# Performance work log

Measured on AMD Instinct MI355X. Metric: run time of the kernel, lower is better.

Reference implementation:

```python
import jax, jax.numpy as jnp
import numpy as np
from jax import lax

B, N, K, NCP = 4, 2048, 20, 400
EPS = 1e-5


def _bn(x, gamma, beta, axes):
    # training-mode batch norm (biased variance), channel axis = 1
    m = jnp.mean(x, axis=axes, keepdims=True)
    v = jnp.var(x, axis=axes, keepdims=True)
    shape = [1] * x.ndim
    shape[1] = -1
    return (x - m) * lax.rsqrt(v + EPS) * gamma.reshape(shape) + beta.reshape(shape)


def _knn_idx(x, k):
    # x: [B, C, N] -> idx [B, N, k] (nearest, includes self like torch.cdist+topk(largest=False))
    x2 = jnp.sum(x * x, axis=1)  # [B, N]
    d = x2[:, :, None] + x2[:, None, :] - 2.0 * jnp.einsum('bcn,bcm->bnm', x, x)
    return lax.top_k(-d, k)[1]


def _edge_conv(x, w, gamma, beta, k):
    # x: [B, C, N], w: [O, 2C] -> [B, O, N] (1x1 conv + BN + LeakyReLU + max over k)
    idx = _knn_idx(x, k)                      # [B, N, k]
    xt = jnp.transpose(x, (0, 2, 1))          # [B, N, C]
    b = jnp.arange(xt.shape[0])[:, None, None]
    nbr = xt[b, idx]                          # [B, N, k, C]
    ctr = xt[:, :, None, :]
    feat = jnp.concatenate([nbr - ctr, jnp.broadcast_to(ctr, nbr.shape)], axis=-1)  # [B, N, k, 2C]
    y = jnp.einsum('bnkc,oc->bonk', feat, w)  # [B, O, N, k]
    y = jax.nn.leaky_relu(_bn(y, gamma, beta, axes=(0, 2, 3)), 0.2)
    return jnp.max(y, axis=-1)                # [B, O, N]


def setup_inputs() -> dict:
    key = jax.random.key(0)
    ks = jax.random.split(key, 16)
    rnd = lambda k_, s: jax.random.normal(k_, s, dtype=jnp.float32) * 0.02
    inp = {
        'x': jax.random.normal(ks[0], (B, 3, N), dtype=jnp.float32),
        'w1': rnd(ks[1], (64, 6)),    'g1': jnp.ones(64),   'b1': jnp.zeros(64),
        'w2': rnd(ks[2], (128, 128)), 'g2': jnp.ones(128),  'b2': jnp.zeros(128),
        'w3': rnd(ks[3], (256, 256)), 'g3': jnp.ones(256),  'b3': jnp.zeros(256),
        'w4': rnd(ks[4], (512, 512)), 'g4': jnp.ones(512),  'b4': jnp.zeros(512),
        'w5': rnd(ks[5], (2048, 963)), 'g5': jnp.ones(2048), 'b5': jnp.zeros(2048),
        'w6': rnd(ks[6], (2048, 2048)), 'wb6': jnp.zeros(2048), 'g6': jnp.ones(2048), 'b6': jnp.zeros(2048),
        'w7': rnd(ks[7], (4096, 4096)), 'wb7': jnp.zeros(4096), 'g7': jnp.ones(4096), 'b7': jnp.zeros(4096),
        'w8': rnd(ks[8], (NCP, 4096)), 'wb8': jnp.zeros(NCP),
    }
    return inp


def reference(x, w1, g1, b1, w2, g2, b2, w3, g3, b3, w4, g4, b4,
              w5, g5, b5, w6, wb6, g6, b6, w7, wb7, g7, b7, w8, wb8):
    x0 = x                                            # [B, 3, N]
    x1 = _edge_conv(x0, w1, g1, b1, K)                # [B, 64, N]
    x2 = _edge_conv(x1, w2, g2, b2, K)                # [B, 128, N]
    x3 = _edge_conv(x2, w3, g3, b3, K)                # [B, 256, N]
    x4 = _edge_conv(x3, w4, g4, b4, K)                # [B, 512, N]
    h = jnp.concatenate([x0, x1, x2, x3, x4], axis=1) # [B, 963, N]
    h = jnp.einsum('bcn,oc->bon', h, w5)              # [B, 2048, N]
    h = jax.nn.leaky_relu(_bn(h, g5, b5, axes=(0, 2)), 0.2)
    p = jnp.max(h, axis=-1, keepdims=True)            # [B, 2048, 1] global max pool
    y = jnp.einsum('bcl,oc->bol', p, w6) + wb6[None, :, None]
    y = jax.nn.relu(_bn(y, g6, b6, axes=(0, 2)))
    y = jnp.concatenate([y, p], axis=1)               # [B, 4096, 1]
    y = jnp.einsum('bcl,oc->bol', y, w7) + wb7[None, :, None]
    y = jax.nn.relu(_bn(y, g7, b7, axes=(0, 2)))
    y = jnp.einsum('bcl,oc->bol', y, w8) + wb8[None, :, None]
    return jnp.tanh(y[:, :, 0])                       # [B, NCP]
```

## Files before the change

### kernel.cpp

```cpp
#include <hip/hip_runtime.h>
#include <float.h>
#include <math.h>


#define NPTS 2048
#define BATCH 4
#define KNN 20
#define CH_H 963
#define KPAD 992
#define HSTRIDE (CH_H*NPTS)

typedef _Float16 half8 __attribute__((ext_vector_type(8)));
typedef float f32x4 __attribute__((ext_vector_type(4)));

typedef const __attribute__((address_space(1))) unsigned int* gas_p;
typedef __attribute__((address_space(3))) unsigned int* las_p;
__device__ __forceinline__ void gl_lds16(const void* g, void* l){
  __builtin_amdgcn_global_load_lds((gas_p)g, (las_p)l, 16, 0, 0);
}

__device__ __forceinline__ unsigned fenc(float x){
  unsigned u = __float_as_uint(x);
  return (u & 0x80000000u) ? ~u : (u | 0x80000000u);
}
__device__ __forceinline__ float fdec(unsigned u){
  u = (u & 0x80000000u) ? (u ^ 0x80000000u) : ~u;
  return __uint_as_float(u);
}

__global__ void k_convert(const float* __restrict__ x, float* __restrict__ H){
  int i = blockIdx.x*256 + threadIdx.x;
  if (i >= BATCH*3*NPTS) return;
  int b = i / (3*NPTS); int r = i % (3*NPTS);
  H[(size_t)b*HSTRIDE + r] = x[i];
}

__global__ void k_norms(const float* __restrict__ X, int C, float* __restrict__ X2,
                        float* __restrict__ SUMZ){
  int i = blockIdx.x*256 + threadIdx.x;
  if (i < 1024) SUMZ[i] = 0.f;
  int b = i >> 11, n = i & 2047;
  const float* Xb = X + (size_t)b*HSTRIDE + n;
  float s = 0.f;
  for (int c=0;c<C;++c){ float v = Xb[(size_t)c*NPTS]; s = fmaf(v,v,s); }
  X2[i] = s;
}

__global__ __launch_bounds__(256) void k_xsplit(const float* __restrict__ X, int C, int Cpad,
        _Float16* __restrict__ Xhi, _Float16* __restrict__ Xlo)
{
  __shared__ float t[64][65];
  int b = blockIdx.z;
  int n0 = blockIdx.x*64, c0 = blockIdx.y*64;
  int tid = threadIdx.x; int l = tid & 63, m = tid >> 6;
  for (int cc = m; cc < 64; cc += 4){
    int c = c0 + cc;
    t[cc][l] = (c < C) ? X[(size_t)b*HSTRIDE + (size_t)c*NPTS + n0 + l] : 0.f;
  }
  __syncthreads();
  for (int nn = m; nn < 64; nn += 4){
    int c = c0 + l;
    if (c < Cpad){
      float v = t[l][nn];
      _Float16 h = (_Float16)v;
      size_t o = ((size_t)(b<<11)+n0+nn)*Cpad + c;
      Xhi[o] = h;
      Xlo[o] = (_Float16)(v - (float)h);
    }
  }
}

__global__ __launch_bounds__(256) void k_gram(const _Float16* __restrict__ Xhi,
        const _Float16* __restrict__ Xlo, int Cpad, int bbase,
        float* __restrict__ G0, float* __restrict__ G1)
{
  __shared__ half8 AsH[128][4]; __shared__ half8 AsL[128][4];
  __shared__ half8 BsH[128][4]; __shared__ half8 BsL[128][4];
  int bl = blockIdx.z;
  int b  = bbase + bl;
  float* G = bl ? G1 : G0;
  const _Float16* Hb = Xhi + (size_t)(b<<11)*Cpad;
  const _Float16* Lb = Xlo + (size_t)(b<<11)*Cpad;
  int m0 = blockIdx.x*128, n0 = blockIdx.y*128;
  int tid = threadIdx.x;
  int w = tid>>6, lane = tid&63;
  int wm = w>>1, wn = w&1;
  int quad = lane>>4, col = lane&15;
  int wbase = w*128;
  f32x4 acc[4][4];
  #pragma unroll
  for (int i=0;i<4;++i)
    #pragma unroll
    for (int j=0;j<4;++j) acc[i][j] = (f32x4){0.f,0.f,0.f,0.f};

  for (int k0=0; k0<Cpad; k0+=32){
    #pragma unroll
    for (int i=0;i<2;++i){
      int cid = wbase + i*64 + lane;
      int row = cid>>2, kc = cid&3;
      size_t ao = (size_t)(n0+row)*Cpad + k0 + kc*8;
      size_t bo = (size_t)(m0+row)*Cpad + k0 + kc*8;
      int lo = (wbase + i*64)*16;
      gl_lds16(Hb + ao, (char*)AsH + lo);
      gl_lds16(Lb + ao, (char*)AsL + lo);
      gl_lds16(Hb + bo, (char*)BsH + lo);
      gl_lds16(Lb + bo, (char*)BsL + lo);
    }
    __syncthreads();
    half8 ah[4], al[4], bh[4], blo[4];
    #pragma unroll
    for (int mt=0;mt<4;++mt){ ah[mt] = AsH[wm*64 + mt*16 + col][quad];
                              al[mt] = AsL[wm*64 + mt*16 + col][quad]; }
    #pragma unroll
    for (int nt=0;nt<4;++nt){ bh[nt] = BsH[wn*64 + nt*16 + col][quad];
                              blo[nt] = BsL[wn*64 + nt*16 + col][quad]; }
    #pragma unroll
    for (int mt=0;mt<4;++mt)
      #pragma unroll
      for (int nt=0;nt<4;++nt){
        acc[mt][nt] = __builtin_amdgcn_mfma_f32_16x16x32_f16(ah[mt], bh[nt], acc[mt][nt], 0, 0, 0);
        acc[mt][nt] = __builtin_amdgcn_mfma_f32_16x16x32_f16(ah[mt], blo[nt], acc[mt][nt], 0, 0, 0);
        acc[mt][nt] = __builtin_amdgcn_mfma_f32_16x16x32_f16(al[mt], bh[nt], acc[mt][nt], 0, 0, 0);
      }
    __syncthreads();
  }
  #pragma unroll
  for (int mt=0;mt<4;++mt){
    #pragma unroll
    for (int r=0;r<4;++r){
      int n = n0 + wm*64 + mt*16 + quad*4 + r;
      #pragma unroll
      for (int nt=0;nt<4;++nt){
        int m = m0 + wn*64 + nt*16 + col;
        G[(size_t)n*2048 + m] = acc[mt][nt][r];
      }
    }
  }
}

#define KNN_CH(OPC) OPC(0) OPC(1) OPC(2) OPC(3) OPC(4) OPC(5) OPC(6) OPC(7)
#define DECL_CH(ch) float d##ch##_0,d##ch##_1,d##ch##_2,d##ch##_3;
#define LOADG_CH(ch) { float4 g = *(const float4*)(grow + (ch)*256 + base); \
  float4 xm = *(const float4*)(x2b + (ch)*256 + base); \
  d##ch##_0 = x2n + xm.x - 2.f*g.x; d##ch##_1 = x2n + xm.y - 2.f*g.y; \
  d##ch##_2 = x2n + xm.z - 2.f*g.z; d##ch##_3 = x2n + xm.w - 2.f*g.w; }
#define DECL_G(ch) float gv##ch; int gm##ch;
#define MKCH(ch) { gv##ch = d##ch##_0; gm##ch = (ch)*256 + base; \
  if (d##ch##_1 < gv##ch){ gv##ch = d##ch##_1; gm##ch = (ch)*256 + base + 1; } \
  if (d##ch##_2 < gv##ch){ gv##ch = d##ch##_2; gm##ch = (ch)*256 + base + 2; } \
  if (d##ch##_3 < gv##ch){ gv##ch = d##ch##_3; gm##ch = (ch)*256 + base + 3; } }
#define REMCASE(ch) case ch: { \
  if (own){ if (cp==0) d##ch##_0 = FLT_MAX; else if (cp==1) d##ch##_1 = FLT_MAX; \
            else if (cp==2) d##ch##_2 = FLT_MAX; else d##ch##_3 = FLT_MAX; } \
  MKCH(ch) } break;

__global__ __launch_bounds__(256,4) void k_sel(const float* __restrict__ G0,
        const float* __restrict__ G1, const float* __restrict__ X2,
        int bbase, int* __restrict__ IDX)
{
  int tid = threadIdx.x;
  int w = tid >> 6, lane = tid & 63;
  int n = blockIdx.x*4 + w;
  int b = bbase + blockIdx.y;
  const float* grow = (blockIdx.y ? G1 : G0) + (size_t)n*2048;
  const float* x2b  = X2 + (b<<11);
  float x2n = x2b[n];
  int base = lane << 2;
  KNN_CH(DECL_CH)
  KNN_CH(LOADG_CH)
  KNN_CH(DECL_G)
  KNN_CH(MKCH)
  int* op = IDX + ((size_t)(b<<11)+n)*KNN;
  for (int it=0; it<KNN; ++it){
    float v = fminf(fminf(fminf(gv0,gv1),fminf(gv2,gv3)),
                    fminf(fminf(gv4,gv5),fminf(gv6,gv7)));
    #pragma unroll
    for (int s=1; s<64; s<<=1) v = fminf(v, __shfl_xor(v, s));
    int mc = 0x7fffffff;
    mc = (gv7==v) ? gm7 : mc;
    mc = (gv6==v) ? gm6 : mc;
    mc = (gv5==v) ? gm5 : mc;
    mc = (gv4==v) ? gm4 : mc;
    mc = (gv3==v) ? gm3 : mc;
    mc = (gv2==v) ? gm2 : mc;
    mc = (gv1==v) ? gm1 : mc;
    mc = (gv0==v) ? gm0 : mc;
    int m = mc;
    #pragma unroll
    for (int s=1; s<64; s<<=1) m = min(m, __shfl_xor(m, s));
    if (lane==0) op[it] = m;
    int sm = __builtin_amdgcn_readfirstlane(m);
    bool own = (lane == ((sm>>2)&63));
    int cp = sm & 3;
    switch (sm >> 8){ KNN_CH(REMCASE) }
  }
}

__global__ __launch_bounds__(256) void k_vu(const float* __restrict__ X,
        const float* __restrict__ W, int C, int O,
        float* __restrict__ V, float* __restrict__ U)
{
  __shared__ float Xs[8][128];
  __shared__ float Wdv[8][64];
  __shared__ float Wuv[8][64];
  int b = blockIdx.z, n0 = blockIdx.x*128, o0 = blockIdx.y*64;
  int tid = threadIdx.x;
  int tj = tid & 15, ti = tid >> 4;
  float4 aV[8], aU[8];
  #pragma unroll
  for (int i=0;i<8;++i){ aV[i]=make_float4(0,0,0,0); aU[i]=make_float4(0,0,0,0); }
  const float* Xb = X + (size_t)b*HSTRIDE;
  for (int c0=0;c0<C;c0+=8){
    {
      int cc = tid >> 5, nn = (tid & 31) * 4; int c = c0 + cc;
      float4 v = (c<C) ? *(const float4*)(Xb + (size_t)c*NPTS + n0 + nn)
                       : make_float4(0,0,0,0);
      *(float4*)&Xs[cc][nn] = v;
    }
    for (int l=tid;l<512;l+=256){
      int oo=l>>3, cc=l&7, c=c0+cc;
      float wd=0.f, wu=0.f;
      if (c<C){
        const float* wr = W + (size_t)(o0+oo)*(2*C);
        wd = wr[c]; wu = wr[C+c] - wd;
      }
      Wdv[cc][oo]=wd; Wuv[cc][oo]=wu;
    }
    __syncthreads();
    #pragma unroll
    for (int cc=0;cc<8;++cc){
      float4 x0 = *(float4*)&Xs[cc][ti*8];
      float4 x1 = *(float4*)&Xs[cc][ti*8+4];
      float4 wd = *(float4*)&Wdv[cc][tj*4];
      float4 wu = *(float4*)&Wuv[cc][tj*4];
      float xs[8] = {x0.x,x0.y,x0.z,x0.w,x1.x,x1.y,x1.z,x1.w};
      #pragma unroll
      for (int i=0;i<8;++i){
        aV[i].x = fmaf(xs[i], wd.x, aV[i].x);
        aV[i].y = fmaf(xs[i], wd.y, aV[i].y);
        aV[i].z = fmaf(xs[i], wd.z, aV[i].z);
        aV[i].w = fmaf(xs[i], wd.w, aV[i].w);
        aU[i].x = fmaf(xs[i], wu.x, aU[i].x);
        aU[i].y = fmaf(xs[i], wu.y, aU[i].y);
        aU[i].z = fmaf(xs[i], wu.z, aU[i].z);
        aU[i].w = fmaf(xs[i], wu.w, aU[i].w);
      }
    }
    __syncthreads();
  }
  #pragma unroll
  for (int i=0;i<8;++i){
    int n = n0 + ti*8 + i;
    size_t basep = ((size_t)b*NPTS + n)*O + o0 + tj*4;
    *(float4*)(V+basep) = aV[i];
    *(float4*)(U+basep) = aU[i];
  }
}

template<int OC, int CHN>
__global__ __launch_bounds__(256) void k_gather(const float* __restrict__ V,
        const float* __restrict__ U, const int* __restrict__ IDX,
        float* __restrict__ YMX, float* __restrict__ YMN,
        float* __restrict__ SUM, float* __restrict__ SUMSQ)
{
  constexpr int O = OC*CHN;
  constexpr int NT = 8;
  constexpr int NSTEP = 256/OC;
  __shared__ int sidx[NT*KNN];
  __shared__ float rs[256], rq[256];
  int bid = blockIdx.x;
  int xcd  = bid & 7;
  int b    = xcd >> 1;
  int half = xcd & 1;
  int r    = bid >> 3;
  int ngrp, chunk;
  if (CHN == 1){ ngrp = (half<<7) | r; chunk = 0; }
  else         { ngrp = r & 255; chunk = half*(CHN/2) + (r>>8); }
  int n0 = ngrp * NT;
  int tid = threadIdx.x;
  for (int l = tid; l < NT*KNN; l += 256)
    sidx[l] = IDX[((size_t)(b<<11)+n0)*KNN + l];
  __syncthreads();
  int o  = chunk*OC + (tid & (OC-1));
  int ns = tid / OC;
  const float* Vb = V + (size_t)(b<<11)*O + o;
  float s = 0.f, q = 0.f;
  #pragma unroll
  for (int i = 0; i < NT/NSTEP; ++i){
    int nn = ns + i*NSTEP;
    int n = n0 + nn;
    size_t ub = ((size_t)(b<<11)+n)*O + o;
    float sv = 0.f, sv2 = 0.f, mx = -FLT_MAX, mn = FLT_MAX;
    #pragma unroll
    for (int k=0;k<KNN;++k){
      int m = sidx[nn*KNN+k];
      float v = Vb[(size_t)m*O];
      mx = fmaxf(mx,v); mn = fminf(mn,v);
      sv += v; sv2 = fmaf(v,v,sv2);
    }
    float u = __builtin_nontemporal_load(U + ub);
    __builtin_nontemporal_store(mx + u, YMX + ub);
    __builtin_nontemporal_store(mn + u, YMN + ub);
    s += sv + (float)KNN * u;
    q += sv2 + 2.f*u*sv + (float)KNN*u*u;
  }
  rs[tid] = s; rq[tid] = q;
  __syncthreads();
  if (tid < OC){
    #pragma unroll
    for (int t=1; t<NSTEP; ++t){ s += rs[tid + t*OC]; q += rq[tid + t*OC]; }
    atomicAdd(&SUM[o], s);
    atomicAdd(&SUMSQ[o], q);
  }
}

__global__ void k_finalize(const float* __restrict__ SUM, const float* __restrict__ SUMSQ,
        const float* __restrict__ g, const float* __restrict__ bt,
        int O, float invM, float* __restrict__ SC, float* __restrict__ SH){
  int o = blockIdx.x*256 + threadIdx.x;
  if (o>=O) return;
  float m = SUM[o]*invM;
  float var = SUMSQ[o]*invM - m*m;
  float sc = g[o] * rsqrtf(var + 1e-5f);
  SC[o]=sc; SH[o] = bt[o] - m*sc;
}

__global__ __launch_bounds__(256) void k_apply(const float* __restrict__ YMX, const float* __restrict__ YMN,
        const float* __restrict__ SC, const float* __restrict__ SH,
        int O, float* __restrict__ OUT)
{
  __shared__ float t[64][65];
  int b = blockIdx.z;
  int o0 = blockIdx.y*64, n0 = blockIdx.x*64;
  int tid = threadIdx.x;
  int lo = tid & 63, ln = tid >> 6;
  float sc = SC[o0+lo], sh = SH[o0+lo];
  for (int nn = ln; nn < 64; nn += 4){
    size_t idx = ((size_t)(b<<11)+n0+nn)*O + o0 + lo;
    float v = (sc >= 0.f) ? YMX[idx] : YMN[idx];
    float y = fmaf(sc, v, sh);
    y = (y > 0.f) ? y : 0.2f*y;
    t[lo][nn] = y;
  }
  __syncthreads();
  for (int oo = ln; oo < 64; oo += 4){
    OUT[(size_t)b*HSTRIDE + (size_t)(o0+oo)*NPTS + n0 + lo] = t[oo][lo];
  }
}

__global__ __launch_bounds__(256) void k_h2f16(const float* __restrict__ H, _Float16* __restrict__ Hf){
  __shared__ float t[64][65];
  int b = blockIdx.z;
  int n0 = blockIdx.x*64, c0 = blockIdx.y*64;
  int tid = threadIdx.x; int l = tid & 63, m = tid >> 6;
  for (int cc = m; cc < 64; cc += 4){
    int c = c0 + cc;
    t[cc][l] = (c < CH_H) ? H[(size_t)b*HSTRIDE + (size_t)c*NPTS + n0 + l] : 0.f;
  }
  __syncthreads();
  for (int nn = m; nn < 64; nn += 4){
    int c = c0 + l;
    if (c < KPAD)
      Hf[((size_t)(b<<11)+n0+nn)*KPAD + c] = (_Float16)t[l][nn];
  }
}

__global__ void k_w5f16(const float* __restrict__ w5, _Float16* __restrict__ Wf,
                        unsigned* __restrict__ z){
  int i = blockIdx.x*256 + threadIdx.x;
  if (i < 12288) z[i] = 0u;
  else if (i < 20480) z[i] = 0xFFFFFFFFu;
  if (i >= 2048*KPAD) return;
  int o = i / KPAD, c = i - o*KPAD;
  Wf[i] = (c < CH_H) ? (_Float16)w5[(size_t)o*CH_H + c] : (_Float16)0.f;
}

__global__ __launch_bounds__(256) void k_l5mfma(const _Float16* __restrict__ Wf,
        const _Float16* __restrict__ Hf,
        float* __restrict__ SUM5, float* __restrict__ SUMSQ5,
        unsigned* __restrict__ MAXB, unsigned* __restrict__ MINB)
{
  __shared__ half8 As[128][4];
  __shared__ half8 Bs[128][4];
  int b  = blockIdx.z;
  int n0 = blockIdx.x*128, o0 = blockIdx.y*128;
  int tid = threadIdx.x;
  int w = tid>>6, lane = tid&63;
  int wm = w>>1, wn = w&1;
  int quad = lane>>4, col = lane&15;
  int wbase = w*128;
  f32x4 acc[4][4];
  #pragma unroll
  for (int i=0;i<4;++i)
    #pragma unroll
    for (int j=0;j<4;++j) acc[i][j] = (f32x4){0.f,0.f,0.f,0.f};

  for (int k0=0; k0<KPAD; k0+=32){
    #pragma unroll
    for (int i=0;i<2;++i){
      int cid = wbase + i*64 + lane;
      int row = cid>>2, kc = cid&3;
      int lo = (wbase + i*64)*16;
      gl_lds16(Wf + (size_t)(o0+row)*KPAD + k0 + kc*8, (char*)As + lo);
      gl_lds16(Hf + ((size_t)(b<<11)+n0+row)*KPAD + k0 + kc*8, (char*)Bs + lo);
    }
    __syncthreads();
    half8 af[4], bf[4];
    #pragma unroll
    for (int mt=0;mt<4;++mt) af[mt] = As[wm*64 + mt*16 + col][quad];
    #pragma unroll
    for (int nt=0;nt<4;++nt) bf[nt] = Bs[wn*64 + nt*16 + col][quad];
    #pragma unroll
    for (int mt=0;mt<4;++mt)
      #pragma unroll
      for (int nt=0;nt<4;++nt)
        acc[mt][nt] = __builtin_amdgcn_mfma_f32_16x16x32_f16(af[mt], bf[nt], acc[mt][nt], 0, 0, 0);
    __syncthreads();
  }
  #pragma unroll
  for (int mt=0;mt<4;++mt){
    #pragma unroll
    for (int r=0;r<4;++r){
      float s=0.f, q=0.f, mx=-FLT_MAX, mn=FLT_MAX;
      #pragma unroll
      for (int nt=0;nt<4;++nt){
        float y = acc[mt][nt][r];
        s += y; q = fmaf(y,y,q);
        mx = fmaxf(mx,y); mn = fminf(mn,y);
      }
      #pragma unroll
      for (int d=8; d; d>>=1){
        s += __shfl_down(s,(unsigned)d,16);
        q += __shfl_down(q,(unsigned)d,16);
        mx = fmaxf(mx,__shfl_down(mx,(unsigned)d,16));
        mn = fminf(mn,__shfl_down(mn,(unsigned)d,16));
      }
      if (col==0){
        int o = o0 + wm*64 + mt*16 + quad*4 + r;
        atomicAdd(&SUM5[o], s);
        atomicAdd(&SUMSQ5[o], q);
        atomicMax(&MAXB[(b<<11)+o], fenc(mx));
        atomicMin(&MINB[(b<<11)+o], fenc(mn));
      }
    }
  }
}

__global__ void k_l5_final(const float* __restrict__ SUM5, const float* __restrict__ SUMSQ5,
        const unsigned* __restrict__ MAXB, const unsigned* __restrict__ MINB,
        const float* __restrict__ g5, const float* __restrict__ b5, float* __restrict__ P)
{
  int o = blockIdx.x*256 + threadIdx.x;
  if (o>=2048) return;
  float m = SUM5[o]*(1.f/8192.f);
  float var = SUMSQ5[o]*(1.f/8192.f) - m*m;
  float sc = g5[o] * rsqrtf(var + 1e-5f);
  float sh = b5[o] - m*sc;
  for (int b=0;b<4;++b){
    float mx = fdec(MAXB[b*2048+o]);
    float mn = fdec(MINB[b*2048+o]);
    float v = (sc >= 0.f) ? fmaf(sc,mx,sh) : fmaf(sc,mn,sh);
    v = (v > 0.f) ? v : 0.2f*v;
    P[b*2048 + o] = v;
  }
}

__global__ __launch_bounds__(256) void k_fc(const float* __restrict__ W, const float* __restrict__ bias,
        const float* __restrict__ Z, int Cin, int O, float* __restrict__ Y)
{
  int o = blockIdx.x*4 + (threadIdx.x>>6);
  int lane = threadIdx.x & 63;
  if (o >= O) return;
  const float* wr = W + (size_t)o*Cin;
  float a0=0.f,a1=0.f,a2=0.f,a3=0.f;
  for (int c=lane;c<Cin;c+=64){
    float w = wr[c];
    a0 = fmaf(w, Z[c],        a0);
    a1 = fmaf(w, Z[Cin+c],    a1);
    a2 = fmaf(w, Z[2*Cin+c],  a2);
    a3 = fmaf(w, Z[3*Cin+c],  a3);
  }
  #pragma unroll
  for (int s=32;s;s>>=1){
    a0 += __shfl_down(a0,(unsigned)s); a1 += __shfl_down(a1,(unsigned)s);
    a2 += __shfl_down(a2,(unsigned)s); a3 += __shfl_down(a3,(unsigned)s);
  }
  if (lane==0){
    float bb = bias[o];
    Y[o]=a0+bb; Y[O+o]=a1+bb; Y[2*O+o]=a2+bb; Y[3*O+o]=a3+bb;
  }
}

__global__ void k_bn4(const float* __restrict__ Y, const float* __restrict__ g, const float* __restrict__ bt,
                      int O, float* __restrict__ Z, int zstride, int zoff)
{
  int o = blockIdx.x*256 + threadIdx.x;
  if (o>=O) return;
  float v0=Y[o], v1=Y[O+o], v2=Y[2*O+o], v3=Y[3*O+o];
  float m = 0.25f*(v0+v1+v2+v3);
  float d0=v0-m, d1=v1-m, d2=v2-m, d3=v3-m;
  float var = 0.25f*(d0*d0+d1*d1+d2*d2+d3*d3);
  float sc = g[o] * rsqrtf(var + 1e-5f);
  float sh = bt[o] - m*sc;
  Z[0*zstride+zoff+o] = fmaxf(fmaf(sc,v0,sh), 0.f);
  Z[1*zstride+zoff+o] = fmaxf(fmaf(sc,v1,sh), 0.f);
  Z[2*zstride+zoff+o] = fmaxf(fmaf(sc,v2,sh), 0.f);
  Z[3*zstride+zoff+o] = fmaxf(fmaf(sc,v3,sh), 0.f);
}

__global__ void k_copy_p(const float* __restrict__ P, float* __restrict__ Z){
  int i = blockIdx.x*256 + threadIdx.x;
  int b = i>>11, o = i&2047;
  Z[b*4096 + 2048 + o] = P[i];
}

__global__ __launch_bounds__(256) void k_final(const float* __restrict__ W8, const float* __restrict__ wb8,
        const float* __restrict__ Z7, float* __restrict__ out)
{
  int o = blockIdx.x*4 + (threadIdx.x>>6);
  int lane = threadIdx.x & 63;
  if (o >= 400) return;
  const float* wr = W8 + (size_t)o*4096;
  float a0=0.f,a1=0.f,a2=0.f,a3=0.f;
  for (int c=lane;c<4096;c+=64){
    float w = wr[c];
    a0 = fmaf(w, Z7[c],        a0);
    a1 = fmaf(w, Z7[4096+c],   a1);
    a2 = fmaf(w, Z7[2*4096+c], a2);
    a3 = fmaf(w, Z7[3*4096+c], a3);
  }
  #pragma unroll
  for (int s=32;s;s>>=1){
    a0 += __shfl_down(a0,(unsigned)s); a1 += __shfl_down(a1,(unsigned)s);
    a2 += __shfl_down(a2,(unsigned)s); a3 += __shfl_down(a3,(unsigned)s);
  }
  if (lane==0){
    float bb = wb8[o];
    out[0*400+o] = tanhf(a0+bb);
    out[1*400+o] = tanhf(a1+bb);
    out[2*400+o] = tanhf(a2+bb);
    out[3*400+o] = tanhf(a3+bb);
  }
}

extern "C" void kernel_launch(void* const* d_in, const int* in_sizes, int n_in,
                              void* d_out, int out_size, void* d_ws, size_t ws_size,
                              hipStream_t stream)
{
  const float* x   = (const float*)d_in[0];
  const float* w_e[4]  = {(const float*)d_in[1], (const float*)d_in[4], (const float*)d_in[7], (const float*)d_in[10]};
  const float* g_e[4]  = {(const float*)d_in[2], (const float*)d_in[5], (const float*)d_in[8], (const float*)d_in[11]};
  const float* b_e[4]  = {(const float*)d_in[3], (const float*)d_in[6], (const float*)d_in[9], (const float*)d_in[12]};
  const float* w5  = (const float*)d_in[13];
  const float* g5  = (const float*)d_in[14];
  const float* b5  = (const float*)d_in[15];
  const float* w6  = (const float*)d_in[16];
  const float* wb6 = (const float*)d_in[17];
  const float* g6  = (const float*)d_in[18];
  const float* b6  = (const float*)d_in[19];
  const float* w7  = (const float*)d_in[20];
  const float* wb7 = (const float*)d_in[21];
  const float* g7  = (const float*)d_in[22];
  const float* b7  = (const float*)d_in[23];
  const float* w8  = (const float*)d_in[24];
  const float* wb8 = (const float*)d_in[25];

  float* WS = (float*)d_ws;
  float* H    = WS;
  float* V    = WS + 7888896;
  float* U    = V  + 4194304;
  float* YMX  = U  + 4194304;
  float* YMN  = YMX+ 4194304;
  int*   IDX  = (int*)(YMN + 4194304);
  float* X2   = (float*)(IDX + 163840);
  float* SUM  = X2 + 8192;
  float* SUMSQ= SUM + 512;
  float* SC   = SUMSQ + 512;
  float* SH   = SC + 512;
  float* SUM5 = SH + 512;
  float* SUMSQ5 = SUM5 + 2048;
  unsigned* MAXB = (unsigned*)(SUMSQ5 + 2048);
  unsigned* MINB = MAXB + 8192;
  float* P    = (float*)(MINB + 8192);
  float* Y6   = P + 8192;
  float* Z    = Y6 + 8192;
  float* Y7   = Z + 16384;
  float* Z7   = Y7 + 16384;
  _Float16* Hf  = (_Float16*)V;
  _Float16* Wf  = (_Float16*)U;
  _Float16* Xhi = (_Float16*)U;
  _Float16* Xlo = (_Float16*)U + 4*2048*256;
  float* G0 = YMX;
  float* G1 = YMN;

  k_convert<<<96,256,0,stream>>>(x, H);

  const int Cin_[4]  = {3,64,128,256};
  const int Cpad_[4] = {32,64,128,256};
  const int O_[4]    = {64,128,256,512};
  const int ioff_[4] = {0,3,67,195};
  const int ooff_[4] = {3,67,195,451};

  for (int l=0;l<4;++l){
    const float* Xl = H + (size_t)ioff_[l]*NPTS;
    int C = Cin_[l], Cpad = Cpad_[l], O = O_[l];
    k_norms<<<32,256,0,stream>>>(Xl, C, X2, SUM);
    dim3 gxs(32, (Cpad+63)/64, 4);
    k_xsplit<<<gxs,256,0,stream>>>(Xl, C, Cpad, Xhi, Xlo);
    dim3 ggr(16,16,2);
    k_gram<<<ggr,256,0,stream>>>(Xhi, Xlo, Cpad, 0, G0, G1);
    dim3 gsl(512,2);
    k_sel<<<gsl,256,0,stream>>>(G0, G1, X2, 0, IDX);
    k_gram<<<ggr,256,0,stream>>>(Xhi, Xlo, Cpad, 2, G0, G1);
    k_sel<<<gsl,256,0,stream>>>(G0, G1, X2, 2, IDX);
    dim3 gvu(16, O/64, 4);
    k_vu<<<gvu,256,0,stream>>>(Xl, w_e[l], C, O, V, U);
    if (O == 64)
      k_gather<64,1><<<1024,256,0,stream>>>(V, U, IDX, YMX, YMN, SUM, SUMSQ);
    else if (O == 128)
      k_gather<128,1><<<1024,256,0,stream>>>(V, U, IDX, YMX, YMN, SUM, SUMSQ);
    else if (O == 256)
      k_gather<128,2><<<2048,256,0,stream>>>(V, U, IDX, YMX, YMN, SUM, SUMSQ);
    else
      k_gather<128,4><<<4096,256,0,stream>>>(V, U, IDX, YMX, YMN, SUM, SUMSQ);
    k_finalize<<<2,256,0,stream>>>(SUM, SUMSQ, g_e[l], b_e[l], O, 1.f/163840.f, SC, SH);
    dim3 gap(32, O/64, 4);
    k_apply<<<gap,256,0,stream>>>(YMX, YMN, SC, SH, O, H + (size_t)ooff_[l]*NPTS);
  }

  dim3 gtr(32,16,4);
  k_h2f16<<<gtr,256,0,stream>>>(H, Hf);
  k_w5f16<<<(2048*KPAD+255)/256,256,0,stream>>>(w5, Wf, (unsigned*)SUM5);
  dim3 g5g(16,16,4);
  k_l5mfma<<<g5g,256,0,stream>>>(Wf, Hf, SUM5, SUMSQ5, MAXB, MINB);
  k_l5_final<<<8,256,0,stream>>>(SUM5, SUMSQ5, MAXB, MINB, g5, b5, P);

  k_fc<<<512,256,0,stream>>>(w6, wb6, P, 2048, 2048, Y6);
  k_bn4<<<8,256,0,stream>>>(Y6, g6, b6, 2048, Z, 4096, 0);
  k_copy_p<<<32,256,0,stream>>>(P, Z);
  k_fc<<<1024,256,0,stream>>>(w7, wb7, Z, 4096, 4096, Y7);
  k_bn4<<<16,256,0,stream>>>(Y7, g7, b7, 4096, Z7, 4096, 0);
  k_final<<<100,256,0,stream>>>(w8, wb8, Z7, (float*)d_out);
}
```

Baseline: 1.086 ms.

## Double-buffer LDS tiles in gram and layer-5 MFMA GEMM kernels

Both the kNN gram kernel and the layer-5 MFMA GEMM now keep two LDS buffers and issue global-to-LDS loads for the next K tile before computing on the current one. This is meant to overlap global memory latency with MFMA work instead of stalling on a barrier right after each load. In exchange, LDS use per block doubles, which may lower occupancy. Correctness depends on the trailing barrier in each loop iteration and on async load completion before that barrier; the prefetch into the other buffer is issued before the current buffer's LDS reads.

```diff
diff --git a/kernel.cpp b/kernel.cpp
--- a/kernel.cpp
+++ b/kernel.cpp
@@ -74,8 +74,8 @@
         const _Float16* __restrict__ Xlo, int Cpad, int bbase,
         float* __restrict__ G0, float* __restrict__ G1)
 {
-  __shared__ half8 AsH[128][4]; __shared__ half8 AsL[128][4];
-  __shared__ half8 BsH[128][4]; __shared__ half8 BsL[128][4];
+  __shared__ half8 AsH[2][128][4]; __shared__ half8 AsL[2][128][4];
+  __shared__ half8 BsH[2][128][4]; __shared__ half8 BsL[2][128][4];
   int bl = blockIdx.z;
   int b  = bbase + bl;
   float* G = bl ? G1 : G0;
@@ -93,7 +93,7 @@
     #pragma unroll
     for (int j=0;j<4;++j) acc[i][j] = (f32x4){0.f,0.f,0.f,0.f};
 
-  for (int k0=0; k0<Cpad; k0+=32){
+  auto stageg = [&](int buf, int k0){
     #pragma unroll
     for (int i=0;i<2;++i){
       int cid = wbase + i*64 + lane;
@@ -101,19 +101,26 @@
       size_t ao = (size_t)(n0+row)*Cpad + k0 + kc*8;
       size_t bo = (size_t)(m0+row)*Cpad + k0 + kc*8;
       int lo = (wbase + i*64)*16;
-      gl_lds16(Hb + ao, (char*)AsH + lo);
-      gl_lds16(Lb + ao, (char*)AsL + lo);
-      gl_lds16(Hb + bo, (char*)BsH + lo);
-      gl_lds16(Lb + bo, (char*)BsL + lo);
-    }
-    __syncthreads();
+      gl_lds16(Hb + ao, (char*)&AsH[buf][0][0] + lo);
+      gl_lds16(Lb + ao, (char*)&AsL[buf][0][0] + lo);
+      gl_lds16(Hb + bo, (char*)&BsH[buf][0][0] + lo);
+      gl_lds16(Lb + bo, (char*)&BsL[buf][0][0] + lo);
+    }
+  };
+
+  int NT = Cpad >> 5;
+  stageg(0, 0);
+  __syncthreads();
+  for (int kt=0; kt<NT; ++kt){
+    int buf = kt & 1;
+    if (kt+1 < NT) stageg(buf^1, (kt+1)<<5);
     half8 ah[4], al[4], bh[4], blo[4];
     #pragma unroll
-    for (int mt=0;mt<4;++mt){ ah[mt] = AsH[wm*64 + mt*16 + col][quad];
-                              al[mt] = AsL[wm*64 + mt*16 + col][quad]; }
-    #pragma unroll
-    for (int nt=0;nt<4;++nt){ bh[nt] = BsH[wn*64 + nt*16 + col][quad];
-                              blo[nt] = BsL[wn*64 + nt*16 + col][quad]; }
+    for (int mt=0;mt<4;++mt){ ah[mt] = AsH[buf][wm*64 + mt*16 + col][quad];
+                              al[mt] = AsL[buf][wm*64 + mt*16 + col][quad]; }
+    #pragma unroll
+    for (int nt=0;nt<4;++nt){ bh[nt] = BsH[buf][wn*64 + nt*16 + col][quad];
+                              blo[nt] = BsL[buf][wn*64 + nt*16 + col][quad]; }
     #pragma unroll
     for (int mt=0;mt<4;++mt)
       #pragma unroll
@@ -380,8 +387,8 @@
         float* __restrict__ SUM5, float* __restrict__ SUMSQ5,
         unsigned* __restrict__ MAXB, unsigned* __restrict__ MINB)
 {
-  __shared__ half8 As[128][4];
-  __shared__ half8 Bs[128][4];
+  __shared__ half8 As[2][128][4];
+  __shared__ half8 Bs[2][128][4];
   int b  = blockIdx.z;
   int n0 = blockIdx.x*128, o0 = blockIdx.y*128;
   int tid = threadIdx.x;
@@ -395,21 +402,28 @@
     #pragma unroll
     for (int j=0;j<4;++j) acc[i][j] = (f32x4){0.f,0.f,0.f,0.f};
 
-  for (int k0=0; k0<KPAD; k0+=32){
+  auto stage5 = [&](int buf, int k0){
     #pragma unroll
     for (int i=0;i<2;++i){
       int cid = wbase + i*64 + lane;
       int row = cid>>2, kc = cid&3;
       int lo = (wbase + i*64)*16;
-      gl_lds16(Wf + (size_t)(o0+row)*KPAD + k0 + kc*8, (char*)As + lo);
-      gl_lds16(Hf + ((size_t)(b<<11)+n0+row)*KPAD + k0 + kc*8, (char*)Bs + lo);
-    }
-    __syncthreads();
+      gl_lds16(Wf + (size_t)(o0+row)*KPAD + k0 + kc*8, (char*)&As[buf][0][0] + lo);
+      gl_lds16(Hf + ((size_t)(b<<11)+n0+row)*KPAD + k0 + kc*8, (char*)&Bs[buf][0][0] + lo);
+    }
+  };
+
+  const int NT = KPAD/32;
+  stage5(0, 0);
+  __syncthreads();
+  for (int kt=0; kt<NT; ++kt){
+    int buf = kt & 1;
+    if (kt+1 < NT) stage5(buf^1, (kt+1)*32);
     half8 af[4], bf[4];
     #pragma unroll
-    for (int mt=0;mt<4;++mt) af[mt] = As[wm*64 + mt*16 + col][quad];
-    #pragma unroll
-    for (int nt=0;nt<4;++nt) bf[nt] = Bs[wn*64 + nt*16 + col][quad];
+    for (int mt=0;mt<4;++mt) af[mt] = As[buf][wm*64 + mt*16 + col][quad];
+    #pragma unroll
+    for (int nt=0;nt<4;++nt) bf[nt] = Bs[buf][wn*64 + nt*16 + col][quad];
     #pragma unroll
     for (int mt=0;mt<4;++mt)
       #pragma unroll
```

Measured after the change: 1.075 ms. No clear change (-1.1%).
